# Kernel optimization log

Measured on AMD Instinct MI355X. Metric: run time of the kernel, lower is better.

Reference implementation:

```python
import jax, jax.numpy as jnp
import numpy as np

B, T, N, D = 8, 12, 883, 128
H, C = 8, 16          # heads, out_channels per head (D = H*C, concat=True)
E = 7000              # edges per graph instance
FF = 2048             # feed_forward_dim
NEG_SLOPE = 0.2       # GATv2Conv default negative_slope


def setup_inputs() -> dict:
    key = jax.random.key(0)
    ks = jax.random.split(key, 16)
    s = 0.05
    return {
        "x": jax.random.normal(ks[0], (B, T, N, D), jnp.float32),
        "edge_index": jax.random.randint(ks[1], (2, E), 0, N, dtype=jnp.int64),
        # GATv2Conv params (lin_l, lin_r each have bias by default; att vector; final bias)
        "Wl": jax.random.normal(ks[2], (D, H * C), jnp.float32) * s,
        "bl": jnp.zeros((H * C,), jnp.float32),
        "Wr": jax.random.normal(ks[3], (D, H * C), jnp.float32) * s,
        "br": jnp.zeros((H * C,), jnp.float32),
        "att": jax.random.normal(ks[4], (H, C), jnp.float32) * s,
        "bias_gat": jnp.zeros((H * C,), jnp.float32),
        # FFN
        "W1": jax.random.normal(ks[5], (D, FF), jnp.float32) * s,
        "b1": jnp.zeros((FF,), jnp.float32),
        "W2": jax.random.normal(ks[6], (FF, D), jnp.float32) * s,
        "b2": jnp.zeros((D,), jnp.float32),
        # LayerNorms
        "g1": jnp.ones((D,), jnp.float32),
        "be1": jnp.zeros((D,), jnp.float32),
        "g2": jnp.ones((D,), jnp.float32),
        "be2": jnp.zeros((D,), jnp.float32),
    }


def _layer_norm(x, g, b, eps=1e-5):
    mu = x.mean(-1, keepdims=True)
    var = ((x - mu) ** 2).mean(-1, keepdims=True)
    return (x - mu) * jax.lax.rsqrt(var + eps) * g + b


def _forward(x, edge_index, Wl, bl, Wr, br, att, bias_gat,
             W1, b1, W2, b2, g1, be1, g2, be2):
    B_, T_, N_, D_ = x.shape
    BT = B_ * T_
    TN = BT * N_
    # expand shared edge_index across B*T instances (per torch code)
    offsets = jnp.arange(BT, dtype=edge_index.dtype) * N_
    ee = (edge_index[None, :, :] + offsets[:, None, None]).transpose(1, 0, 2).reshape(2, -1)
    # PyG GATv2Conv default: add self loops
    loops = jnp.arange(TN, dtype=edge_index.dtype)
    src = jnp.concatenate([ee[0], loops])  # message source j
    dst = jnp.concatenate([ee[1], loops])  # message target i

    xf = x.reshape(TN, D_)
    x_l = (xf @ Wl + bl).reshape(TN, H, C)
    x_r = (xf @ Wr + br).reshape(TN, H, C)

    # GATv2 attention: leaky_relu(x_l[j] + x_r[i]) . att
    e = x_l[src] + x_r[dst]                        # [Etot, H, C]
    e = jnp.where(e > 0, e, NEG_SLOPE * e)
    score = jnp.einsum('ehc,hc->eh', e, att)       # [Etot, H]

    # segment softmax over incoming edges per target node
    smax = jax.ops.segment_max(score, dst, num_segments=TN)
    a = jnp.exp(score - smax[dst])
    denom = jax.ops.segment_sum(a, dst, num_segments=TN)
    alpha = a / denom[dst]                          # [Etot, H]

    # scatter-add aggregation of alpha * x_l[src]
    agg = jax.ops.segment_sum(alpha[:, :, None] * x_l[src], dst, num_segments=TN)
    x_gat = (agg.reshape(TN, H * C) + bias_gat).reshape(B_, T_, N_, D_)

    h = _layer_norm(x + x_gat, g1, be1)
    ff = (jnp.maximum(h.reshape(-1, D_) @ W1 + b1, 0.0) @ W2 + b2).reshape(h.shape)
    return _layer_norm(h + ff, g2, be2)


def reference(x, edge_index, Wl, bl, Wr, br, att, bias_gat,
              W1, b1, W2, b2, g1, be1, g2, be2):
    return _forward(x, edge_index, Wl, bl, Wr, br, att, bias_gat,
                    W1, b1, W2, b2, g1, be1, g2, be2)
```

## Files before the change

kernel.cpp:

```cpp
#include <hip/hip_runtime.h>
#include <stdint.h>

typedef unsigned short u16;

#define TN    84768
#define NNODE 883
#define DD    128
#define EE    7000
#define FFDIM 2048

typedef short bf16x8 __attribute__((ext_vector_type(8)));
typedef float f32x4  __attribute__((ext_vector_type(4)));
typedef __attribute__((address_space(3))) u16 lds_u16;
typedef const __attribute__((address_space(1))) u16 glb_u16;

__device__ __forceinline__ float bf2f(u16 u) {
    unsigned int x = ((unsigned int)u) << 16;
    return __uint_as_float(x);
}
__device__ __forceinline__ u16 f2bf(float f) {
    unsigned int x = __float_as_uint(f);
    x += 0x7FFFu + ((x >> 16) & 1u);
    return (u16)(x >> 16);
}
__device__ __forceinline__ u16 cleanu(u16 u) {
    return (((u >> 7) & 0xFF) == 0xFF) ? (u16)0 : u;
}
__device__ __forceinline__ u16 cleanf(float f) {
    unsigned b = __float_as_uint(f);
    if (((b >> 23) & 0xFF) == 0xFF) return 0;
    return cleanu(f2bf(f));
}

__global__ __launch_bounds__(256) void k_detect(const unsigned* __restrict__ x,
                                                int* __restrict__ flag) {
    __shared__ int cnt;
    if (threadIdx.x == 0) cnt = 0;
    __syncthreads();
    unsigned w = x[threadIdx.x];
    unsigned e = (w >> 7) & 0xFF;
    int ok = (e >= 96 && e <= 144) || ((w & 0xFFFFu) == 0);
    atomicAdd(&cnt, ok);
    __syncthreads();
    if (threadIdx.x == 0) flag[0] = (cnt < 200) ? 1 : 0;
}

__global__ __launch_bounds__(256) void k_prep(const void* Wl, const void* Wr,
                                              const void* W1, const void* W2,
                                              const void* bl, const void* br,
                                              const void* att, const void* bgat,
                                              const void* b1, const void* b2,
                                              const void* g1, const void* be1,
                                              const void* g2, const void* be2,
                                              u16* __restrict__ wlrT,
                                              u16* __restrict__ w1T,
                                              u16* __restrict__ w2T,
                                              u16* __restrict__ canon,
                                              const int* __restrict__ flag) {
    int f32 = *flag;
    int i = blockIdx.x * 256 + threadIdx.x;
    if (i < 16384) {
        int r = i >> 7, c = i & 127;
        u16 v = f32 ? cleanf(((const float*)Wl)[i]) : cleanu(((const u16*)Wl)[i]);
        wlrT[c * 128 + r] = v;
    } else if (i < 32768) {
        int idx = i - 16384;
        int r = idx >> 7, c = idx & 127;
        u16 v = f32 ? cleanf(((const float*)Wr)[idx]) : cleanu(((const u16*)Wr)[idx]);
        wlrT[16384 + c * 128 + r] = v;
    } else if (i < 294912) {
        int idx = i - 32768;
        int r = idx >> 11, c = idx & 2047;
        u16 v = f32 ? cleanf(((const float*)W1)[idx]) : cleanu(((const u16*)W1)[idx]);
        w1T[c * 128 + r] = v;
    } else if (i < 557056) {
        int idx = i - 294912;
        int r = idx >> 7, c = idx & 127;
        u16 v = f32 ? cleanf(((const float*)W2)[idx]) : cleanu(((const u16*)W2)[idx]);
        w2T[c * 2048 + r] = v;
    } else if (i < 560256) {
        int p = i - 557056;
        const void* src; int off;
        if      (p < 128)  { src = bl;   off = 0; }
        else if (p < 256)  { src = br;   off = 128; }
        else if (p < 384)  { src = att;  off = 256; }
        else if (p < 512)  { src = bgat; off = 384; }
        else if (p < 2560) { src = b1;   off = 512; }
        else if (p < 2688) { src = b2;   off = 2560; }
        else if (p < 2816) { src = g1;   off = 2688; }
        else if (p < 2944) { src = be1;  off = 2816; }
        else if (p < 3072) { src = g2;   off = 2944; }
        else               { src = be2;  off = 3072; }
        int j = p - off;
        canon[p] = f32 ? cleanf(((const float*)src)[j]) : cleanu(((const u16*)src)[j]);
    }
}

__global__ __launch_bounds__(1024) void k_csr(const int* __restrict__ ew,
                                              int* __restrict__ row_off,
                                              int* __restrict__ col) {
    __shared__ int cnt[NNODE];
    __shared__ int offs[NNODE + 1];
    __shared__ int cur[NNODE];
    __shared__ int flag;
    int tid = threadIdx.x;
    if (tid == 0) flag = 0;
    for (int i = tid; i < NNODE; i += 1024) cnt[i] = 0;
    __syncthreads();
    int f = 0;
    for (int j = tid; j < EE; j += 1024) f |= ew[2 * j + 1];
    if (f) atomicOr(&flag, 1);
    __syncthreads();
    bool is32 = (flag != 0);
    for (int e = tid; e < EE; e += 1024) {
        int dst = is32 ? ew[EE + e] : ew[2 * EE + 2 * e];
        if ((unsigned)dst < NNODE) atomicAdd(&cnt[dst], 1);
    }
    __syncthreads();
    if (tid == 0) {
        int run = 0;
        for (int i = 0; i < NNODE; ++i) { offs[i] = run; run += cnt[i]; }
        offs[NNODE] = run;
    }
    __syncthreads();
    for (int i = tid; i < NNODE; i += 1024) cur[i] = offs[i];
    __syncthreads();
    for (int e = tid; e < EE; e += 1024) {
        int src = is32 ? ew[e] : ew[2 * e];
        int dst = is32 ? ew[EE + e] : ew[2 * EE + 2 * e];
        if ((unsigned)dst < NNODE && (unsigned)src < NNODE) {
            int p = atomicAdd(&cur[dst], 1);
            if (p < EE) col[p] = src;
        }
    }
    __syncthreads();
    for (int i = tid; i <= NNODE; i += 1024) row_off[i] = offs[i];
}

__global__ __launch_bounds__(256) void k_linlr(const void* __restrict__ xraw,
                                               const u16* __restrict__ wlrT,
                                               const u16* __restrict__ canon,
                                               u16* __restrict__ xl, u16* __restrict__ xr,
                                               const int* __restrict__ flag) {
    __shared__ __align__(16) u16 a_tile[64 * 136];
    int f32 = *flag;
    int tid = threadIdx.x;
    int m0 = blockIdx.x * 64;
    for (int it = 0; it < 4; ++it) {
        int idx = it * 256 + tid;
        int row = idx >> 4, cc = idx & 15;
        int gm = m0 + row;
        u16 tmp[8];
#pragma unroll
        for (int j = 0; j < 8; ++j) tmp[j] = 0;
        if (gm < TN) {
            size_t base = (size_t)gm * DD + cc * 8;
            if (f32) {
                float4 v0 = *(const float4*)((const float*)xraw + base);
                float4 v1 = *(const float4*)((const float*)xraw + base + 4);
                tmp[0] = cleanf(v0.x); tmp[1] = cleanf(v0.y);
                tmp[2] = cleanf(v0.z); tmp[3] = cleanf(v0.w);
                tmp[4] = cleanf(v1.x); tmp[5] = cleanf(v1.y);
                tmp[6] = cleanf(v1.z); tmp[7] = cleanf(v1.w);
            } else {
                uint4 v = *(const uint4*)((const u16*)xraw + base);
                unsigned wv[4] = {v.x, v.y, v.z, v.w};
#pragma unroll
                for (int j = 0; j < 8; ++j)
                    tmp[j] = cleanu((u16)((wv[j >> 1] >> ((j & 1) * 16)) & 0xFFFFu));
            }
        }
        uint4 o;
        o.x = (unsigned)tmp[0] | ((unsigned)tmp[1] << 16);
        o.y = (unsigned)tmp[2] | ((unsigned)tmp[3] << 16);
        o.z = (unsigned)tmp[4] | ((unsigned)tmp[5] << 16);
        o.w = (unsigned)tmp[6] | ((unsigned)tmp[7] << 16);
        *(uint4*)(a_tile + row * 136 + cc * 8) = o;
    }
    __syncthreads();
    int wave = tid >> 6, lane = tid & 63, n16 = lane & 15, q = lane >> 4;
    f32x4 acc[16];
#pragma unroll
    for (int t = 0; t < 16; ++t) acc[t] = (f32x4){0, 0, 0, 0};
    const u16* arow = a_tile + (16 * wave + n16) * 136;
#pragma unroll
    for (int ks = 0; ks < 4; ++ks) {
        bf16x8 a = *(const bf16x8*)(arow + ks * 32 + q * 8);
#pragma unroll
        for (int t = 0; t < 16; ++t) {
            bf16x8 b = *(const bf16x8*)(wlrT + ((size_t)(t * 16 + n16)) * DD + ks * 32 + q * 8);
            acc[t] = __builtin_amdgcn_mfma_f32_16x16x32_bf16(a, b, acc[t], 0, 0, 0);
        }
    }
#pragma unroll
    for (int t = 0; t < 16; ++t) {
        int cc = (t & 7) * 16 + n16;
        float bias = bf2f(canon[(t < 8 ? 0 : 128) + cc]);
        u16* dst = (t < 8 ? xl : xr);
#pragma unroll
        for (int reg = 0; reg < 4; ++reg) {
            int mrow = m0 + 16 * wave + 4 * q + reg;
            if (mrow < TN) dst[(size_t)mrow * DD + cc] = f2bf(acc[t][reg] + bias);
        }
    }
}

__device__ __forceinline__ float segsum16(float p) {
    p += __shfl_xor(p, 1, 16);
    p += __shfl_xor(p, 2, 16);
    p += __shfl_xor(p, 4, 16);
    p += __shfl_xor(p, 8, 16);
    return p;
}

__global__ __launch_bounds__(256) void k_gat(const void* __restrict__ xraw,
                                             const u16* __restrict__ xl,
                                             const u16* xr,
                                             const u16* __restrict__ canon,
                                             const int* __restrict__ row_off,
                                             const int* __restrict__ col,
                                             u16* h1,
                                             const int* __restrict__ flag) {
    int f32 = *flag;
    int tid = threadIdx.x;
    int wave = tid >> 6, lane = tid & 63;
    int g = blockIdx.x * 4 + wave;
    int bt = g / NNODE;
    int i = g - bt * NNODE;
    size_t gbase = (size_t)g * DD;
    const u16* xlrow0 = xl + (size_t)bt * NNODE * DD;
    int c2 = lane * 2;
    unsigned uxr = *(const unsigned*)(xr + gbase + c2);
    float xr0 = __uint_as_float(uxr << 16);
    float xr1 = __uint_as_float(uxr & 0xFFFF0000u);
    unsigned uat = *(const unsigned*)(canon + 256 + c2);
    float at0 = __uint_as_float(uat << 16);
    float at1 = __uint_as_float(uat & 0xFFFF0000u);
    unsigned uxs = *(const unsigned*)(xl + gbase + c2);
    float xs0 = __uint_as_float(uxs << 16);
    float xs1 = __uint_as_float(uxs & 0xFFFF0000u);
    float t0 = xs0 + xr0, t1 = xs1 + xr1;
    t0 = fmaxf(t0, 0.2f * t0); t1 = fmaxf(t1, 0.2f * t1);
    float p = t0 * at0 + t1 * at1;
    p += __shfl_xor(p, 1, 8);
    p += __shfl_xor(p, 2, 8);
    p += __shfl_xor(p, 4, 8);
    p = fminf(fmaxf(p, -30.f), 30.f);
    float w = __expf(p);
    float denom = w;
    float a0 = w * xs0, a1 = w * xs1;
    int r0 = row_off[i], r1 = row_off[i + 1];
    for (int e = r0; e < r1; ++e) {
        int j = __builtin_amdgcn_readfirstlane(col[e]);
        if ((unsigned)j >= NNODE) continue;
        unsigned uj = *(const unsigned*)(xlrow0 + (size_t)j * DD + c2);
        float x0 = __uint_as_float(uj << 16);
        float x1 = __uint_as_float(uj & 0xFFFF0000u);
        float u0 = x0 + xr0, u1 = x1 + xr1;
        u0 = fmaxf(u0, 0.2f * u0); u1 = fmaxf(u1, 0.2f * u1);
        float q = u0 * at0 + u1 * at1;
        q += __shfl_xor(q, 1, 8);
        q += __shfl_xor(q, 2, 8);
        q += __shfl_xor(q, 4, 8);
        q = fminf(fmaxf(q, -30.f), 30.f);
        float ww = __expf(q);
        denom += ww;
        a0 += ww * x0;
        a1 += ww * x1;
    }
    float inv = 1.f / denom;
    unsigned ubg = *(const unsigned*)(canon + 384 + c2);
    float res0, res1;
    if (f32) {
        float2 rr = *(const float2*)((const float*)xraw + gbase + c2);
        unsigned b0 = __float_as_uint(rr.x), b1 = __float_as_uint(rr.y);
        res0 = (((b0 >> 23) & 0xFF) == 0xFF) ? 0.f : rr.x;
        res1 = (((b1 >> 23) & 0xFF) == 0xFF) ? 0.f : rr.y;
    } else {
        unsigned ux = *(const unsigned*)((const u16*)xraw + gbase + c2);
        res0 = bf2f(cleanu((u16)(ux & 0xFFFFu)));
        res1 = bf2f(cleanu((u16)(ux >> 16)));
    }
    float pre0 = a0 * inv + __uint_as_float(ubg << 16) + res0;
    float pre1 = a1 * inv + __uint_as_float(ubg & 0xFFFF0000u) + res1;
    float sum = pre0 + pre1, sq = pre0 * pre0 + pre1 * pre1;
    for (int off = 32; off; off >>= 1) {
        sum += __shfl_xor(sum, off);
        sq  += __shfl_xor(sq, off);
    }
    float mu = sum * (1.0f / 128.0f);
    float var = fmaxf(sq * (1.0f / 128.0f) - mu * mu, 0.f);
    float rs = rsqrtf(var + 1e-5f);
    unsigned ug = *(const unsigned*)(canon + 2688 + c2);
    unsigned ub = *(const unsigned*)(canon + 2816 + c2);
    float h0 = (pre0 - mu) * rs * __uint_as_float(ug << 16) + __uint_as_float(ub << 16);
    float h1v = (pre1 - mu) * rs * __uint_as_float(ug & 0xFFFF0000u) + __uint_as_float(ub & 0xFFFF0000u);
    unsigned out = (unsigned)f2bf(h0) | ((unsigned)f2bf(h1v) << 16);
    *(unsigned*)(h1 + gbase + c2) = out;
}

__global__ __launch_bounds__(256, 3) void k_ffn(const u16* __restrict__ h1,
                                                const u16* __restrict__ w1T,
                                                const u16* __restrict__ w2T,
                                                const u16* __restrict__ canon,
                                                void* __restrict__ outraw,
                                                const int* __restrict__ flag) {
    __shared__ __align__(16) u16 w1b[64 * 128];
    __shared__ __align__(16) u16 w2b[128 * 64];
    __shared__ __align__(16) u16 s_t[128 * 72];
    int f32 = *flag;
    int tid = threadIdx.x;
    int wave = tid >> 6, lane = tid & 63, n16 = lane & 15, q = lane >> 4;
    int m0 = blockIdx.x * 128;
    int swz = n16 & 7;
    bf16x8 af[2][4];
#pragma unroll
    for (int sub = 0; sub < 2; ++sub) {
        int gm = m0 + 32 * wave + 16 * sub + n16;
#pragma unroll
        for (int ks = 0; ks < 4; ++ks) {
            if (gm < TN) {
                uint4 v = *(const uint4*)(h1 + (size_t)gm * DD + ks * 32 + q * 8);
                af[sub][ks] = *(const bf16x8*)&v;
            } else {
                uint4 z = make_uint4(0, 0, 0, 0);
                af[sub][ks] = *(const bf16x8*)&z;
            }
        }
    }
    f32x4 acc2[2][8];
#pragma unroll
    for (int sub = 0; sub < 2; ++sub)
#pragma unroll
        for (int t = 0; t < 8; ++t) acc2[sub][t] = (f32x4){0, 0, 0, 0};
    int w1r[4], w1b_log[4];
#pragma unroll
    for (int i = 0; i < 4; ++i) {
        w1r[i] = 16 * wave + 4 * i + (lane >> 4);
        w1b_log[i] = (lane & 15) ^ (w1r[i] & 7);
    }
    int w2r[4], w2b_log[4];
#pragma unroll
    for (int i = 0; i < 4; ++i) {
        w2r[i] = 32 * wave + 8 * i + (lane >> 3);
        w2b_log[i] = (lane & 7) ^ (w2r[i] & 7);
    }
    u16* srow_w0 = s_t + (32 * wave + 4 * q) * 72;
    u16* srow_w1 = s_t + (32 * wave + 16 + 4 * q) * 72;
    const u16* srow_r0 = s_t + (32 * wave + n16) * 72;
    const u16* srow_r1 = s_t + (32 * wave + 16 + n16) * 72;
    for (int ch = 0; ch < 32; ++ch) {
        int f0 = ch * 64;
        __syncthreads();
#pragma unroll
        for (int i = 0; i < 4; ++i) {
            glb_u16* g1 = (glb_u16*)(w1T + (size_t)(f0 + w1r[i]) * DD + w1b_log[i] * 8);
            lds_u16* l1 = (lds_u16*)(w1b + (16 * wave + 4 * i) * 128);
            __builtin_amdgcn_global_load_lds((const __attribute__((address_space(1))) unsigned*)g1,
                                             (__attribute__((address_space(3))) unsigned*)l1,
                                             16, 0, 0);
        }
#pragma unroll
        for (int i = 0; i < 4; ++i) {
            glb_u16* g2 = (glb_u16*)(w2T + (size_t)w2r[i] * FFDIM + f0 + w2b_log[i] * 8);
            lds_u16* l2 = (lds_u16*)(w2b + (32 * wave + 8 * i) * 64);
            __builtin_amdgcn_global_load_lds((const __attribute__((address_space(1))) unsigned*)g2,
                                             (__attribute__((address_space(3))) unsigned*)l2,
                                             16, 0, 0);
        }
        __syncthreads();
#pragma unroll
        for (int t = 0; t < 4; ++t) {
            f32x4 a10 = (f32x4){0, 0, 0, 0};
            f32x4 a11 = (f32x4){0, 0, 0, 0};
#pragma unroll
            for (int ks = 0; ks < 4; ++ks) {
                bf16x8 b = *(const bf16x8*)(w1b + (t * 16 + n16) * 128 + (((ks * 4 + q) ^ swz) * 8));
                a10 = __builtin_amdgcn_mfma_f32_16x16x32_bf16(af[0][ks], b, a10, 0, 0, 0);
                a11 = __builtin_amdgcn_mfma_f32_16x16x32_bf16(af[1][ks], b, a11, 0, 0, 0);
            }
            float bb = bf2f(canon[512 + f0 + t * 16 + n16]);
#pragma unroll
            for (int reg = 0; reg < 4; ++reg) {
                float v0 = a10[reg] + bb;
                float v1 = a11[reg] + bb;
                v0 = v0 > 0.f ? v0 : 0.f;
                v1 = v1 > 0.f ? v1 : 0.f;
                srow_w0[reg * 72 + t * 16 + n16] = f2bf(v0);
                srow_w1[reg * 72 + t * 16 + n16] = f2bf(v1);
            }
        }
        asm volatile("" ::: "memory");
#pragma unroll
        for (int ks2 = 0; ks2 < 2; ++ks2) {
            bf16x8 a20 = *(const bf16x8*)(srow_r0 + ks2 * 32 + q * 8);
            bf16x8 a21 = *(const bf16x8*)(srow_r1 + ks2 * 32 + q * 8);
#pragma unroll
            for (int t = 0; t < 8; ++t) {
                bf16x8 b = *(const bf16x8*)(w2b + (t * 16 + n16) * 64 + (((ks2 * 4 + q) ^ swz) * 8));
                acc2[0][t] = __builtin_amdgcn_mfma_f32_16x16x32_bf16(a20, b, acc2[0][t], 0, 0, 0);
                acc2[1][t] = __builtin_amdgcn_mfma_f32_16x16x32_bf16(a21, b, acc2[1][t], 0, 0, 0);
            }
        }
        asm volatile("" ::: "memory");
    }
    float b2v[8], g2v[8], e2v[8];
#pragma unroll
    for (int t = 0; t < 8; ++t) {
        int col = t * 16 + n16;
        b2v[t] = bf2f(canon[2560 + col]);
        g2v[t] = bf2f(canon[2944 + col]);
        e2v[t] = bf2f(canon[3072 + col]);
    }
#pragma unroll
    for (int sub = 0; sub < 2; ++sub) {
#pragma unroll
        for (int reg = 0; reg < 4; ++reg) {
            int row = 32 * wave + 16 * sub + 4 * q + reg;
            int gm = m0 + row;
            bool ok = gm < TN;
            size_t gb = (size_t)(ok ? gm : 0) * DD;
            float v[8]; float s1 = 0.f, s2 = 0.f;
#pragma unroll
            for (int t = 0; t < 8; ++t) {
                float hres = bf2f(h1[gb + t * 16 + n16]);
                v[t] = acc2[sub][t][reg] + b2v[t] + hres;
                s1 += v[t]; s2 += v[t] * v[t];
            }
            s1 = segsum16(s1);
            s2 = segsum16(s2);
            float mu = s1 * (1.f / 128.f);
            float var = fmaxf(s2 * (1.f / 128.f) - mu * mu, 0.f);
            float rs = rsqrtf(var + 1e-5f);
            if (ok) {
#pragma unroll
                for (int t = 0; t < 8; ++t) {
                    float r = (v[t] - mu) * rs * g2v[t] + e2v[t];
                    if (f32) ((float*)outraw)[gb + t * 16 + n16] = r;
                    else     ((u16*)outraw)[gb + t * 16 + n16] = f2bf(r);
                }
            }
        }
    }
}

extern "C" void kernel_launch(void* const* d_in, const int* in_sizes, int n_in,
                              void* d_out, int out_size, void* d_ws, size_t ws_size,
                              hipStream_t stream) {
    const void* x    = d_in[0];
    const int* eidx  = (const int*)d_in[1];
    const void* Wl   = d_in[2];
    const void* bl   = d_in[3];
    const void* Wr   = d_in[4];
    const void* br   = d_in[5];
    const void* att  = d_in[6];
    const void* bgat = d_in[7];
    const void* W1   = d_in[8];
    const void* b1   = d_in[9];
    const void* W2   = d_in[10];
    const void* b2   = d_in[11];
    const void* g1   = d_in[12];
    const void* be1  = d_in[13];
    const void* g2   = d_in[14];
    const void* be2  = d_in[15];

    char* ws = (char*)d_ws;
    int* flag   = (int*)(ws);
    int* rowoff = (int*)(ws + 4096);
    int* colw   = (int*)(ws + 8192);
    u16* canon  = (u16*)(ws + 36864);
    u16* wlrT   = (u16*)(ws + 65536);
    u16* w1T    = (u16*)(ws + 131072);
    u16* w2T    = (u16*)(ws + 655360);
    u16* xl     = (u16*)(ws + 1179648);
    u16* xr     = (u16*)(ws + 22880256);
    u16* h1     = xr;

    k_csr<<<1, 1024, 0, stream>>>(eidx, rowoff, colw);
    k_detect<<<1, 256, 0, stream>>>((const unsigned*)x, flag);
    k_prep<<<2189, 256, 0, stream>>>(Wl, Wr, W1, W2, bl, br, att, bgat, b1, b2,
                                     g1, be1, g2, be2, wlrT, w1T, w2T, canon, flag);
    k_linlr<<<(TN + 63) / 64, 256, 0, stream>>>(x, wlrT, canon, xl, xr, flag);
    k_gat<<<TN / 4, 256, 0, stream>>>(x, xl, xr, canon, rowoff, colw, h1, flag);
    k_ffn<<<(TN + 127) / 128, 256, 0, stream>>>(h1, w1T, w2T, canon, d_out, flag);
}
```

Measured before the change: 399.4 us.

## Double-buffer FFN weight chunks and prefetch neighbor rows in GAT aggregation

The FFN kernel now streams W1/W2 in 32-wide chunks through two LDS buffers, issuing the next chunk's global-to-LDS loads before computing the current one and waiting with vmcnt. This hides weight-load latency behind the MFMAs instead of serialising load, barrier and compute. The GAT edge loop now loads neighbor indices once per wave via shuffle and software-pipelines the neighbor row loads two edges ahead. The cost is more barriers per output (64 chunks instead of 32) and extra register pressure.

```diff
diff --git a/kernel.cpp b/kernel.cpp
--- a/kernel.cpp
+++ b/kernel.cpp
@@ -250,24 +250,54 @@
     float denom = w;
     float a0 = w * xs0, a1 = w * xs1;
     int r0 = row_off[i], r1 = row_off[i + 1];
-    for (int e = r0; e < r1; ++e) {
-        int j = __builtin_amdgcn_readfirstlane(col[e]);
-        if ((unsigned)j >= NNODE) continue;
-        unsigned uj = *(const unsigned*)(xlrow0 + (size_t)j * DD + c2);
-        float x0 = __uint_as_float(uj << 16);
-        float x1 = __uint_as_float(uj & 0xFFFF0000u);
-        float u0 = x0 + xr0, u1 = x1 + xr1;
-        u0 = fmaxf(u0, 0.2f * u0); u1 = fmaxf(u1, 0.2f * u1);
-        float q = u0 * at0 + u1 * at1;
-        q += __shfl_xor(q, 1, 8);
-        q += __shfl_xor(q, 2, 8);
-        q += __shfl_xor(q, 4, 8);
-        q = fminf(fmaxf(q, -30.f), 30.f);
-        float ww = __expf(q);
-        denom += ww;
-        a0 += ww * x0;
-        a1 += ww * x1;
-    }
+    int deg = r1 - r0;
+    int myj = (lane < deg) ? col[r0 + lane] : 0;
+
+#define NEXTJ(kk) __builtin_amdgcn_readfirstlane(((kk) < 64) ? __shfl(myj, (kk)) : col[r0 + (kk)])
+#define EDGE(uvar, okv) do {                                             \
+        float _x0 = __uint_as_float((uvar) << 16);                       \
+        float _x1 = __uint_as_float((uvar) & 0xFFFF0000u);               \
+        float _u0 = _x0 + xr0, _u1 = _x1 + xr1;                          \
+        _u0 = fmaxf(_u0, 0.2f * _u0); _u1 = fmaxf(_u1, 0.2f * _u1);      \
+        float _q = _u0 * at0 + _u1 * at1;                                \
+        _q += __shfl_xor(_q, 1, 8);                                      \
+        _q += __shfl_xor(_q, 2, 8);                                      \
+        _q += __shfl_xor(_q, 4, 8);                                      \
+        _q = fminf(fmaxf(_q, -30.f), 30.f);                              \
+        float _w = (okv) ? __expf(_q) : 0.f;                             \
+        denom += _w; a0 += _w * _x0; a1 += _w * _x1;                     \
+    } while (0)
+
+    unsigned uA = 0, uB = 0;
+    bool okA = false, okB = false;
+    if (deg > 0) {
+        int j = NEXTJ(0); okA = ((unsigned)j < NNODE);
+        uA = *(const unsigned*)(xlrow0 + (size_t)(okA ? j : 0) * DD + c2);
+    }
+    if (deg > 1) {
+        int j = NEXTJ(1); okB = ((unsigned)j < NNODE);
+        uB = *(const unsigned*)(xlrow0 + (size_t)(okB ? j : 0) * DD + c2);
+    }
+    int k = 0;
+    while (k + 1 < deg) {
+        unsigned u = uA; bool ok = okA;
+        if (k + 2 < deg) {
+            int j = NEXTJ(k + 2); okA = ((unsigned)j < NNODE);
+            uA = *(const unsigned*)(xlrow0 + (size_t)(okA ? j : 0) * DD + c2);
+        }
+        EDGE(u, ok);
+        u = uB; ok = okB;
+        if (k + 3 < deg) {
+            int j = NEXTJ(k + 3); okB = ((unsigned)j < NNODE);
+            uB = *(const unsigned*)(xlrow0 + (size_t)(okB ? j : 0) * DD + c2);
+        }
+        EDGE(u, ok);
+        k += 2;
+    }
+    if (k < deg) EDGE(uA, okA);
+#undef EDGE
+#undef NEXTJ
+
     float inv = 1.f / denom;
     unsigned ubg = *(const unsigned*)(canon + 384 + c2);
     float res0, res1;
@@ -305,14 +335,15 @@
                                                 const u16* __restrict__ canon,
                                                 void* __restrict__ outraw,
                                                 const int* __restrict__ flag) {
-    __shared__ __align__(16) u16 w1b[64 * 128];
-    __shared__ __align__(16) u16 w2b[128 * 64];
-    __shared__ __align__(16) u16 s_t[128 * 72];
+    __shared__ __align__(16) u16 w1b[2][32 * 128];
+    __shared__ __align__(16) u16 w2b[2][128 * 32];
+    __shared__ __align__(16) u16 s_t[128 * 40];
     int f32 = *flag;
     int tid = threadIdx.x;
     int wave = tid >> 6, lane = tid & 63, n16 = lane & 15, q = lane >> 4;
     int m0 = blockIdx.x * 128;
     int swz = n16 & 7;
+    int sz2 = (n16 & 3) ^ (n16 >> 2);
     bf16x8 af[2][4];
 #pragma unroll
     for (int sub = 0; sub < 2; ++sub) {
@@ -333,49 +364,61 @@
     for (int sub = 0; sub < 2; ++sub)
 #pragma unroll
         for (int t = 0; t < 8; ++t) acc2[sub][t] = (f32x4){0, 0, 0, 0};
-    int w1r[4], w1b_log[4];
-#pragma unroll
-    for (int i = 0; i < 4; ++i) {
-        w1r[i] = 16 * wave + 4 * i + (lane >> 4);
-        w1b_log[i] = (lane & 15) ^ (w1r[i] & 7);
-    }
-    int w2r[4], w2b_log[4];
-#pragma unroll
-    for (int i = 0; i < 4; ++i) {
-        w2r[i] = 32 * wave + 8 * i + (lane >> 3);
-        w2b_log[i] = (lane & 7) ^ (w2r[i] & 7);
-    }
-    u16* srow_w0 = s_t + (32 * wave + 4 * q) * 72;
-    u16* srow_w1 = s_t + (32 * wave + 16 + 4 * q) * 72;
-    const u16* srow_r0 = s_t + (32 * wave + n16) * 72;
-    const u16* srow_r1 = s_t + (32 * wave + 16 + n16) * 72;
-    for (int ch = 0; ch < 32; ++ch) {
-        int f0 = ch * 64;
-        __syncthreads();
-#pragma unroll
-        for (int i = 0; i < 4; ++i) {
-            glb_u16* g1 = (glb_u16*)(w1T + (size_t)(f0 + w1r[i]) * DD + w1b_log[i] * 8);
-            lds_u16* l1 = (lds_u16*)(w1b + (16 * wave + 4 * i) * 128);
-            __builtin_amdgcn_global_load_lds((const __attribute__((address_space(1))) unsigned*)g1,
-                                             (__attribute__((address_space(3))) unsigned*)l1,
-                                             16, 0, 0);
-        }
-#pragma unroll
-        for (int i = 0; i < 4; ++i) {
-            glb_u16* g2 = (glb_u16*)(w2T + (size_t)w2r[i] * FFDIM + f0 + w2b_log[i] * 8);
-            lds_u16* l2 = (lds_u16*)(w2b + (32 * wave + 8 * i) * 64);
-            __builtin_amdgcn_global_load_lds((const __attribute__((address_space(1))) unsigned*)g2,
-                                             (__attribute__((address_space(3))) unsigned*)l2,
-                                             16, 0, 0);
-        }
-        __syncthreads();
-#pragma unroll
-        for (int t = 0; t < 4; ++t) {
+    const u16 *p1a, *p1b, *p2a, *p2b;
+    {
+        int r0 = 8 * wave + (lane >> 4);
+        int cb0 = (lane & 15) ^ (r0 & 7);
+        p1a = w1T + (size_t)r0 * 128 + cb0 * 8;
+        int r1 = r0 + 4;
+        int cb1 = (lane & 15) ^ (r1 & 7);
+        p1b = w1T + (size_t)r1 * 128 + cb1 * 8;
+        int s0 = 32 * wave + (lane >> 2);
+        int sc0 = (lane & 3) ^ (((lane >> 2) & 3) ^ (lane >> 4));
+        p2a = w2T + (size_t)s0 * 2048 + sc0 * 8;
+        int s1 = s0 + 16;
+        int sc1 = (lane & 3) ^ (((lane >> 2) & 3) ^ (lane >> 4));
+        p2b = w2T + (size_t)s1 * 2048 + sc1 * 8;
+    }
+#define STAGE(f0v, buf) do {                                                          \
+        __builtin_amdgcn_global_load_lds(                                             \
+            (const __attribute__((address_space(1))) unsigned*)(p1a + (size_t)(f0v) * 128), \
+            (__attribute__((address_space(3))) unsigned*)(lds_u16*)&w1b[buf][(8 * wave) * 128], 16, 0, 0); \
+        __builtin_amdgcn_global_load_lds(                                             \
+            (const __attribute__((address_space(1))) unsigned*)(p1b + (size_t)(f0v) * 128), \
+            (__attribute__((address_space(3))) unsigned*)(lds_u16*)&w1b[buf][(8 * wave + 4) * 128], 16, 0, 0); \
+        __builtin_amdgcn_global_load_lds(                                             \
+            (const __attribute__((address_space(1))) unsigned*)(p2a + (f0v)),         \
+            (__attribute__((address_space(3))) unsigned*)(lds_u16*)&w2b[buf][(32 * wave) * 32], 16, 0, 0); \
+        __builtin_amdgcn_global_load_lds(                                             \
+            (const __attribute__((address_space(1))) unsigned*)(p2b + (f0v)),         \
+            (__attribute__((address_space(3))) unsigned*)(lds_u16*)&w2b[buf][(32 * wave + 16) * 32], 16, 0, 0); \
+    } while (0)
+
+    u16* sw0 = s_t + (32 * wave + 4 * q) * 40;
+    u16* sw1 = sw0 + 16 * 40;
+    const u16* sr0 = s_t + (32 * wave + n16) * 40;
+    const u16* sr1 = sr0 + 16 * 40;
+
+    STAGE(0, 0);
+    for (int ch = 0; ch < 64; ++ch) {
+        int cur = ch & 1;
+        if (ch + 1 < 64) {
+            STAGE((ch + 1) * 32, cur ^ 1);
+            asm volatile("s_waitcnt vmcnt(4)" ::: "memory");
+        } else {
+            asm volatile("s_waitcnt vmcnt(0)" ::: "memory");
+        }
+        __builtin_amdgcn_s_barrier();
+        int f0 = ch * 32;
+        const u16* w1c = &w1b[cur][0];
+        const u16* w2c = &w2b[cur][0];
+#pragma unroll
+        for (int t = 0; t < 2; ++t) {
             f32x4 a10 = (f32x4){0, 0, 0, 0};
             f32x4 a11 = (f32x4){0, 0, 0, 0};
 #pragma unroll
             for (int ks = 0; ks < 4; ++ks) {
-                bf16x8 b = *(const bf16x8*)(w1b + (t * 16 + n16) * 128 + (((ks * 4 + q) ^ swz) * 8));
+                bf16x8 b = *(const bf16x8*)(w1c + (t * 16 + n16) * 128 + (((ks * 4 + q) ^ swz) * 8));
                 a10 = __builtin_amdgcn_mfma_f32_16x16x32_bf16(af[0][ks], b, a10, 0, 0, 0);
                 a11 = __builtin_amdgcn_mfma_f32_16x16x32_bf16(af[1][ks], b, a11, 0, 0, 0);
             }
@@ -386,24 +429,22 @@
                 float v1 = a11[reg] + bb;
                 v0 = v0 > 0.f ? v0 : 0.f;
                 v1 = v1 > 0.f ? v1 : 0.f;
-                srow_w0[reg * 72 + t * 16 + n16] = f2bf(v0);
-                srow_w1[reg * 72 + t * 16 + n16] = f2bf(v1);
+                sw0[reg * 40 + t * 16 + n16] = f2bf(v0);
+                sw1[reg * 40 + t * 16 + n16] = f2bf(v1);
             }
         }
         asm volatile("" ::: "memory");
-#pragma unroll
-        for (int ks2 = 0; ks2 < 2; ++ks2) {
-            bf16x8 a20 = *(const bf16x8*)(srow_r0 + ks2 * 32 + q * 8);
-            bf16x8 a21 = *(const bf16x8*)(srow_r1 + ks2 * 32 + q * 8);
-#pragma unroll
-            for (int t = 0; t < 8; ++t) {
-                bf16x8 b = *(const bf16x8*)(w2b + (t * 16 + n16) * 64 + (((ks2 * 4 + q) ^ swz) * 8));
-                acc2[0][t] = __builtin_amdgcn_mfma_f32_16x16x32_bf16(a20, b, acc2[0][t], 0, 0, 0);
-                acc2[1][t] = __builtin_amdgcn_mfma_f32_16x16x32_bf16(a21, b, acc2[1][t], 0, 0, 0);
-            }
-        }
-        asm volatile("" ::: "memory");
-    }
+        bf16x8 a20 = *(const bf16x8*)(sr0 + q * 8);
+        bf16x8 a21 = *(const bf16x8*)(sr1 + q * 8);
+#pragma unroll
+        for (int t = 0; t < 8; ++t) {
+            bf16x8 b = *(const bf16x8*)(w2c + (t * 16 + n16) * 32 + ((q ^ sz2) * 8));
+            acc2[0][t] = __builtin_amdgcn_mfma_f32_16x16x32_bf16(a20, b, acc2[0][t], 0, 0, 0);
+            acc2[1][t] = __builtin_amdgcn_mfma_f32_16x16x32_bf16(a21, b, acc2[1][t], 0, 0, 0);
+        }
+        __builtin_amdgcn_s_barrier();
+    }
+#undef STAGE
     float b2v[8], g2v[8], e2v[8];
 #pragma unroll
     for (int t = 0; t < 8; ++t) {
```

After: 383.3 us. 1.04x faster.

## Process eight edges per wave in parallel in GAT aggregation, parallel CSR scan

Applied to the files above, without the earlier changes.

The GAT kernel now splits each wave into eight lane groups. Each group handles a different incoming edge (self-loop included) and each lane covers 16 channels with 128-bit loads, instead of walking edges serially with every lane holding 2 channels. Partial softmax denominators and weighted sums are merged with cross-group shuffles, and one group then runs the residual and LayerNorm epilogue. The CSR build replaces its single-thread prefix sum with a block-wide Hillis-Steele scan. The cost is more registers per lane, more shuffles, and seven of eight groups sitting idle during the epilogue.

```diff
diff --git a/kernel.cpp b/kernel.cpp
--- a/kernel.cpp
+++ b/kernel.cpp
@@ -30,6 +30,12 @@
     unsigned b = __float_as_uint(f);
     if (((b >> 23) & 0xFF) == 0xFF) return 0;
     return cleanu(f2bf(f));
+}
+__device__ __forceinline__ void unpk8(uint4 v, float* o) {
+    o[0] = __uint_as_float(v.x << 16); o[1] = __uint_as_float(v.x & 0xFFFF0000u);
+    o[2] = __uint_as_float(v.y << 16); o[3] = __uint_as_float(v.y & 0xFFFF0000u);
+    o[4] = __uint_as_float(v.z << 16); o[5] = __uint_as_float(v.z & 0xFFFF0000u);
+    o[6] = __uint_as_float(v.w << 16); o[7] = __uint_as_float(v.w & 0xFFFF0000u);
 }
 
 __global__ __launch_bounds__(256) void k_detect(const unsigned* __restrict__ x,
@@ -102,6 +108,7 @@
     __shared__ int cnt[NNODE];
     __shared__ int offs[NNODE + 1];
     __shared__ int cur[NNODE];
+    __shared__ int sc[1024];
     __shared__ int flag;
     int tid = threadIdx.x;
     if (tid == 0) flag = 0;
@@ -117,11 +124,16 @@
         if ((unsigned)dst < NNODE) atomicAdd(&cnt[dst], 1);
     }
     __syncthreads();
-    if (tid == 0) {
-        int run = 0;
-        for (int i = 0; i < NNODE; ++i) { offs[i] = run; run += cnt[i]; }
-        offs[NNODE] = run;
-    }
+    sc[tid] = (tid < NNODE) ? cnt[tid] : 0;
+    __syncthreads();
+    for (int off = 1; off < 1024; off <<= 1) {
+        int add = (tid >= off) ? sc[tid - off] : 0;
+        __syncthreads();
+        sc[tid] += add;
+        __syncthreads();
+    }
+    if (tid < NNODE) offs[tid] = (tid == 0) ? 0 : sc[tid - 1];
+    if (tid == 0) offs[NNODE] = sc[NNODE - 1];
     __syncthreads();
     for (int i = tid; i < NNODE; i += 1024) cur[i] = offs[i];
     __syncthreads();
@@ -228,75 +240,130 @@
     int bt = g / NNODE;
     int i = g - bt * NNODE;
     size_t gbase = (size_t)g * DD;
-    const u16* xlrow0 = xl + (size_t)bt * NNODE * DD;
-    int c2 = lane * 2;
-    unsigned uxr = *(const unsigned*)(xr + gbase + c2);
-    float xr0 = __uint_as_float(uxr << 16);
-    float xr1 = __uint_as_float(uxr & 0xFFFF0000u);
-    unsigned uat = *(const unsigned*)(canon + 256 + c2);
-    float at0 = __uint_as_float(uat << 16);
-    float at1 = __uint_as_float(uat & 0xFFFF0000u);
-    unsigned uxs = *(const unsigned*)(xl + gbase + c2);
-    float xs0 = __uint_as_float(uxs << 16);
-    float xs1 = __uint_as_float(uxs & 0xFFFF0000u);
-    float t0 = xs0 + xr0, t1 = xs1 + xr1;
-    t0 = fmaxf(t0, 0.2f * t0); t1 = fmaxf(t1, 0.2f * t1);
-    float p = t0 * at0 + t1 * at1;
-    p += __shfl_xor(p, 1, 8);
-    p += __shfl_xor(p, 2, 8);
-    p += __shfl_xor(p, 4, 8);
-    p = fminf(fmaxf(p, -30.f), 30.f);
-    float w = __expf(p);
-    float denom = w;
-    float a0 = w * xs0, a1 = w * xs1;
+    const u16* xl_inst = xl + (size_t)bt * NNODE * DD;
+    int grp = lane >> 3;
+    int cbase = (lane & 7) * 16;
+
+    float at[16], xrv[16];
+    {
+        uint4 a0 = *(const uint4*)(canon + 256 + cbase);
+        uint4 a1 = *(const uint4*)(canon + 256 + cbase + 8);
+        unpk8(a0, at); unpk8(a1, at + 8);
+        uint4 r0v = *(const uint4*)(xr + gbase + cbase);
+        uint4 r1v = *(const uint4*)(xr + gbase + cbase + 8);
+        unpk8(r0v, xrv); unpk8(r1v, xrv + 8);
+    }
+    float acc[16];
+#pragma unroll
+    for (int k = 0; k < 16; ++k) acc[k] = 0.f;
+    float denom = 0.f;
+
     int r0 = row_off[i], r1 = row_off[i + 1];
-    for (int e = r0; e < r1; ++e) {
-        int j = __builtin_amdgcn_readfirstlane(col[e]);
-        if ((unsigned)j >= NNODE) continue;
-        unsigned uj = *(const unsigned*)(xlrow0 + (size_t)j * DD + c2);
-        float x0 = __uint_as_float(uj << 16);
-        float x1 = __uint_as_float(uj & 0xFFFF0000u);
-        float u0 = x0 + xr0, u1 = x1 + xr1;
-        u0 = fmaxf(u0, 0.2f * u0); u1 = fmaxf(u1, 0.2f * u1);
-        float q = u0 * at0 + u1 * at1;
-        q += __shfl_xor(q, 1, 8);
-        q += __shfl_xor(q, 2, 8);
-        q += __shfl_xor(q, 4, 8);
-        q = fminf(fmaxf(q, -30.f), 30.f);
-        float ww = __expf(q);
-        denom += ww;
-        a0 += ww * x0;
-        a1 += ww * x1;
-    }
-    float inv = 1.f / denom;
-    unsigned ubg = *(const unsigned*)(canon + 384 + c2);
-    float res0, res1;
-    if (f32) {
-        float2 rr = *(const float2*)((const float*)xraw + gbase + c2);
-        unsigned b0 = __float_as_uint(rr.x), b1 = __float_as_uint(rr.y);
-        res0 = (((b0 >> 23) & 0xFF) == 0xFF) ? 0.f : rr.x;
-        res1 = (((b1 >> 23) & 0xFF) == 0xFF) ? 0.f : rr.y;
-    } else {
-        unsigned ux = *(const unsigned*)((const u16*)xraw + gbase + c2);
-        res0 = bf2f(cleanu((u16)(ux & 0xFFFFu)));
-        res1 = bf2f(cleanu((u16)(ux >> 16)));
-    }
-    float pre0 = a0 * inv + __uint_as_float(ubg << 16) + res0;
-    float pre1 = a1 * inv + __uint_as_float(ubg & 0xFFFF0000u) + res1;
-    float sum = pre0 + pre1, sq = pre0 * pre0 + pre1 * pre1;
-    for (int off = 32; off; off >>= 1) {
-        sum += __shfl_xor(sum, off);
-        sq  += __shfl_xor(sq, off);
-    }
-    float mu = sum * (1.0f / 128.0f);
-    float var = fmaxf(sq * (1.0f / 128.0f) - mu * mu, 0.f);
-    float rs = rsqrtf(var + 1e-5f);
-    unsigned ug = *(const unsigned*)(canon + 2688 + c2);
-    unsigned ub = *(const unsigned*)(canon + 2816 + c2);
-    float h0 = (pre0 - mu) * rs * __uint_as_float(ug << 16) + __uint_as_float(ub << 16);
-    float h1v = (pre1 - mu) * rs * __uint_as_float(ug & 0xFFFF0000u) + __uint_as_float(ub & 0xFFFF0000u);
-    unsigned out = (unsigned)f2bf(h0) | ((unsigned)f2bf(h1v) << 16);
-    *(unsigned*)(h1 + gbase + c2) = out;
+    int nit = (r1 - r0) + 1;
+    for (int base = 0; base < nit; base += 8) {
+        int item = base + grp;
+        bool valid = item < nit;
+        int j;
+        if (item == 0) {
+            j = i;
+        } else {
+            int eidx = valid ? (r0 + item - 1) : r0;
+            j = col[eidx];
+        }
+        bool okj = valid && ((unsigned)j < NNODE);
+        int jc = okj ? j : 0;
+        const u16* rowp = xl_inst + (size_t)jc * DD + cbase;
+        uint4 v0 = *(const uint4*)(rowp);
+        uint4 v1 = *(const uint4*)(rowp + 8);
+        float xv[16];
+        unpk8(v0, xv); unpk8(v1, xv + 8);
+        float p = 0.f;
+#pragma unroll
+        for (int k = 0; k < 16; ++k) {
+            float u = xv[k] + xrv[k];
+            u = fmaxf(u, 0.2f * u);
+            p = fmaf(u, at[k], p);
+        }
+        p = fminf(fmaxf(p, -30.f), 30.f);
+        float w = okj ? __expf(p) : 0.f;
+        denom += w;
+#pragma unroll
+        for (int k = 0; k < 16; ++k) acc[k] = fmaf(w, xv[k], acc[k]);
+    }
+    denom += __shfl_xor(denom, 8);
+    denom += __shfl_xor(denom, 16);
+    denom += __shfl_xor(denom, 32);
+#pragma unroll
+    for (int k = 0; k < 16; ++k) {
+        acc[k] += __shfl_xor(acc[k], 8);
+        acc[k] += __shfl_xor(acc[k], 16);
+        acc[k] += __shfl_xor(acc[k], 32);
+    }
+    if (grp == 0) {
+        float inv = 1.f / denom;
+        float bg[16];
+        {
+            uint4 b0 = *(const uint4*)(canon + 384 + cbase);
+            uint4 b1 = *(const uint4*)(canon + 384 + cbase + 8);
+            unpk8(b0, bg); unpk8(b1, bg + 8);
+        }
+        float res[16];
+        if (f32) {
+            const float* xp = (const float*)xraw + gbase + cbase;
+            float4 q0 = *(const float4*)(xp);
+            float4 q1 = *(const float4*)(xp + 4);
+            float4 q2 = *(const float4*)(xp + 8);
+            float4 q3 = *(const float4*)(xp + 12);
+            float rr[16] = {q0.x,q0.y,q0.z,q0.w, q1.x,q1.y,q1.z,q1.w,
+                            q2.x,q2.y,q2.z,q2.w, q3.x,q3.y,q3.z,q3.w};
+#pragma unroll
+            for (int k = 0; k < 16; ++k) {
+                unsigned b = __float_as_uint(rr[k]);
+                res[k] = (((b >> 23) & 0xFF) == 0xFF) ? 0.f : rr[k];
+            }
+        } else {
+            const u16* xp = (const u16*)xraw + gbase + cbase;
+            uint4 x0 = *(const uint4*)(xp);
+            uint4 x1 = *(const uint4*)(xp + 8);
+            unsigned wv[8] = {x0.x,x0.y,x0.z,x0.w, x1.x,x1.y,x1.z,x1.w};
+#pragma unroll
+            for (int m = 0; m < 8; ++m) {
+                res[2*m]   = bf2f(cleanu((u16)(wv[m] & 0xFFFFu)));
+                res[2*m+1] = bf2f(cleanu((u16)(wv[m] >> 16)));
+            }
+        }
+        float pre[16];
+        float s1 = 0.f, s2 = 0.f;
+#pragma unroll
+        for (int k = 0; k < 16; ++k) {
+            pre[k] = acc[k] * inv + bg[k] + res[k];
+            s1 += pre[k]; s2 += pre[k] * pre[k];
+        }
+        s1 += __shfl_xor(s1, 1, 8); s2 += __shfl_xor(s2, 1, 8);
+        s1 += __shfl_xor(s1, 2, 8); s2 += __shfl_xor(s2, 2, 8);
+        s1 += __shfl_xor(s1, 4, 8); s2 += __shfl_xor(s2, 4, 8);
+        float mu = s1 * (1.0f / 128.0f);
+        float var = fmaxf(s2 * (1.0f / 128.0f) - mu * mu, 0.f);
+        float rs = rsqrtf(var + 1e-5f);
+        float gv[16], bv[16];
+        {
+            uint4 g0 = *(const uint4*)(canon + 2688 + cbase);
+            uint4 g1v = *(const uint4*)(canon + 2688 + cbase + 8);
+            unpk8(g0, gv); unpk8(g1v, gv + 8);
+            uint4 e0 = *(const uint4*)(canon + 2816 + cbase);
+            uint4 e1 = *(const uint4*)(canon + 2816 + cbase + 8);
+            unpk8(e0, bv); unpk8(e1, bv + 8);
+        }
+        unsigned outw[8];
+#pragma unroll
+        for (int m = 0; m < 8; ++m) {
+            float h0 = (pre[2*m]   - mu) * rs * gv[2*m]   + bv[2*m];
+            float h1v = (pre[2*m+1] - mu) * rs * gv[2*m+1] + bv[2*m+1];
+            outw[m] = (unsigned)f2bf(h0) | ((unsigned)f2bf(h1v) << 16);
+        }
+        *(uint4*)(h1 + gbase + cbase)     = make_uint4(outw[0], outw[1], outw[2], outw[3]);
+        *(uint4*)(h1 + gbase + cbase + 8) = make_uint4(outw[4], outw[5], outw[6], outw[7]);
+    }
 }
 
 __global__ __launch_bounds__(256, 3) void k_ffn(const u16* __restrict__ h1,
```

After: 397.5 us. No clear change (-0.5%).
